# Performance work log

Hardware: AMD Instinct MI355X
Metric: run time of the kernel (lower is better)

Reference implementation:

```python
import jax, jax.numpy as jnp
from jax import lax
import numpy as np

B = 32768      # batch
D = 256        # input = hidden = output dim
DEPTH = 9      # universal_depth


def setup_inputs() -> dict:
    key = jax.random.key(0)
    ks = jax.random.split(key, 16)
    s = 1.0 / np.sqrt(D)  # keep pre-activations sane
    r = lambda k, shp, sc=s: (jax.random.normal(k, shp, jnp.float32) * sc)
    return {
        "x": jax.random.normal(ks[0], (B, D), jnp.float32),
        "lin0_w": r(ks[1], (D, D)), "lin0_b": r(ks[2], (D,), 0.1),
        "lin1_w": r(ks[3], (D, D)), "lin1_b": r(ks[4], (D,), 0.1),
        "u1_w": jax.random.normal(ks[5], (DEPTH, D, D), jnp.float32),
        "u1_cw": r(ks[6], (D, D)), "u1_cb": r(ks[7], (D,), 0.1),
        "lin2_w": r(ks[8], (D, D)), "lin2_b": r(ks[9], (D,), 0.1),
        "u2_w": jax.random.normal(ks[10], (DEPTH, D, D), jnp.float32),
        "u2_cw": r(ks[11], (D, D)), "u2_cb": r(ks[12], (D,), 0.1),
        "lino_w": r(ks[13], (D, D)), "lino_b": r(ks[14], (D,), 0.1),
    }


def _universal_layer(x, uw, cw, cb):
    """UniversalNeuralLayer.forward, vectorized.

    The circulant 'gate' matrix implements, for state s of length n:
        s'[i] = cos*s[i] - sin*s[(i+1)%n] + sin*s[(i-1)%n]
    Applied 3 times per depth with angles uw[d, j, 0..2] (j = output unit).
    The result is independent of x and of the batch index.
    """
    n = x.shape[1]
    classical = x @ cw + cb                      # [B, n]
    # angle sequence per output j, in (depth, gate) order -> [3*DEPTH, n]
    angles = jnp.transpose(uw[:, :, :3], (0, 2, 1)).reshape(-1, n)
    init = jnp.full((n, n), 1.0 / np.sqrt(n), dtype=x.dtype)  # [n_j, n_state]

    def step(s, ang):
        c = jnp.cos(ang)[:, None]
        sn = jnp.sin(ang)[:, None]
        return c * s + sn * (jnp.roll(s, 1, axis=1) - jnp.roll(s, -1, axis=1)), None

    s, _ = lax.scan(step, init, angles)
    p = s[:, 0] ** 2                             # |state[0]|^2 per output j
    return jnp.tanh(classical + p[None, :])


def reference(x, lin0_w, lin0_b, lin1_w, lin1_b, u1_w, u1_cw, u1_cb,
              lin2_w, lin2_b, u2_w, u2_cw, u2_cb, lino_w, lino_b):
    h = jax.nn.relu(x @ lin0_w.T + lin0_b)
    h = jax.nn.relu(h @ lin1_w.T + lin1_b)
    h = _universal_layer(h, u1_w, u1_cw, u1_cb)
    h = jax.nn.relu(h @ lin2_w.T + lin2_b)
    h = _universal_layer(h, u2_w, u2_cw, u2_cb)
    return jax.nn.relu(h @ lino_w.T + lino_b)
```

## Files before the change

kernel.cpp:

```cpp
#include <hip/hip_runtime.h>
#include <math.h>

#define DD 256

typedef float  f32x4  __attribute__((ext_vector_type(4)));
typedef short  bf16x8 __attribute__((ext_vector_type(8)));

__device__ __forceinline__ unsigned short f2bf(float f) {
    unsigned int u = __float_as_uint(f);
    u = (u + 0x7fffu + ((u >> 16) & 1u)) >> 16;
    return (unsigned short)u;
}
__device__ __forceinline__ float bf2f(unsigned int h16) {
    return __uint_as_float(h16 << 16);
}

__global__ __launch_bounds__(256)
void universal_p_kernel(const float* __restrict__ u1_w,
                        const float* __restrict__ u2_w,
                        float* __restrict__ p_out ) {
    const int j = threadIdx.x;
    const float* uw = blockIdx.x ? u2_w : u1_w;
    float s = 0.0625f;
#pragma unroll
    for (int d = 0; d < 9; ++d)
#pragma unroll
        for (int g = 0; g < 3; ++g)
            s *= cosf(uw[d * DD * DD + j * DD + g]);
    p_out[blockIdx.x * DD + j] = s * s;
}

__global__ __launch_bounds__(256)
void prep_weights(const float* __restrict__ w0, const float* __restrict__ w1,
                  const float* __restrict__ cw1, const float* __restrict__ w2,
                  const float* __restrict__ cw2, const float* __restrict__ wo,
                  unsigned short* __restrict__ wall) {
    const int gid  = blockIdx.x * 256 + threadIdx.x;
    const int mat  = gid >> 13;
    const int rem  = gid & 8191;
    const int wb   = rem >> 11;
    const int rem2 = rem & 2047;
    const int k0   = rem2 >> 8;
    const int rem3 = rem2 & 255;
    const int nt   = rem3 >> 6;
    const int lane = rem3 & 63;
    const int n  = wb * 64 + nt * 16 + (lane & 15);
    const int kb = k0 * 32 + (lane >> 4) * 8;

    const float* src;
    bool tr = false;
    switch (mat) {
        case 0: src = w0; break;
        case 1: src = w1; break;
        case 2: src = cw1; tr = true; break;
        case 3: src = w2; break;
        case 4: src = cw2; tr = true; break;
        default: src = wo; break;
    }
    unsigned short tmp[8];
#pragma unroll
    for (int j = 0; j < 8; ++j) {
        const float v = tr ? src[(kb + j) * DD + n] : src[n * DD + kb + j];
        tmp[j] = f2bf(v);
    }
    *(uint4*)&wall[mat * 65536 + wb * 16384 + k0 * 2048 + nt * 512 + lane * 8] =
        *(const uint4*)tmp;
}

__device__ __forceinline__ int chunk_idx(int m, int kc) {
    return kc * 32 + (m ^ (kc & 7));
}

__device__ __forceinline__ float fast_tanh(float x) {
    const float e = __expf(2.0f * x);
    return 1.0f - 2.0f * __builtin_amdgcn_rcpf(1.0f + e);
}

template <int MODE>
__device__ __forceinline__ void layer_step(uint4* h, bf16x8 (&wr)[2][4],
                                           const unsigned short* __restrict__ W,
                                           const unsigned short* __restrict__ Wn,
                                           const float* __restrict__ bias,
                                           const float* __restrict__ pv) {
    const int tid  = threadIdx.x;
    const int wave = tid >> 6;
    const int lane = tid & 63;
    const int quad = lane >> 4;
    const int l15  = lane & 15;
    const unsigned short* Wb  = W  + wave * 16384 + lane * 8;
    const unsigned short* Wnb = Wn + wave * 16384 + lane * 8;

    f32x4 acc[4][2];
#pragma unroll
    for (int nt = 0; nt < 4; ++nt)
#pragma unroll
        for (int mt = 0; mt < 2; ++mt) acc[nt][mt] = (f32x4){0.f, 0.f, 0.f, 0.f};

    bf16x8 h_f[2][2];
#pragma unroll
    for (int mt = 0; mt < 2; ++mt)
        h_f[0][mt] = *(const bf16x8*)&h[chunk_idx(mt * 16 + l15, quad)];

#pragma unroll
    for (int k0 = 0; k0 < 8; ++k0) {
        const int cur = k0 & 1, nxt = cur ^ 1;
        {
            const unsigned short* ws = (k0 < 7) ? &Wb[(k0 + 1) * 2048] : Wnb;
#pragma unroll
            for (int nt = 0; nt < 4; ++nt)
                wr[nxt][nt] = *(const bf16x8*)&ws[nt * 512];
        }
        if (k0 < 7) {
            const int kc = (k0 + 1) * 4 + quad;
#pragma unroll
            for (int mt = 0; mt < 2; ++mt)
                h_f[nxt][mt] = *(const bf16x8*)&h[chunk_idx(mt * 16 + l15, kc)];
        }
#pragma unroll
        for (int nt = 0; nt < 4; ++nt)
#pragma unroll
            for (int mt = 0; mt < 2; ++mt)
                acc[nt][mt] = __builtin_amdgcn_mfma_f32_16x16x32_bf16(
                    wr[cur][nt], h_f[cur][mt], acc[nt][mt], 0, 0, 0);
    }

    __syncthreads();

    const int nb = wave * 64;
#pragma unroll
    for (int nt = 0; nt < 4; ++nt) {
        const int n0 = nb + nt * 16 + quad * 4;
        f32x4 add = *(const f32x4*)&bias[n0];
        if (MODE == 1) add += *(const f32x4*)&pv[n0];
        const int kc_o = n0 >> 3;
        const int half = quad & 1;
#pragma unroll
        for (int mt = 0; mt < 2; ++mt) {
            const f32x4 v = acc[nt][mt] + add;
            float t0, t1, t2, t3;
            if (MODE == 1) {
                t0 = fast_tanh(v.x); t1 = fast_tanh(v.y);
                t2 = fast_tanh(v.z); t3 = fast_tanh(v.w);
            } else {
                t0 = fmaxf(v.x, 0.f); t1 = fmaxf(v.y, 0.f);
                t2 = fmaxf(v.z, 0.f); t3 = fmaxf(v.w, 0.f);
            }
            uint2 u;
            u.x = (unsigned int)f2bf(t0) | ((unsigned int)f2bf(t1) << 16);
            u.y = (unsigned int)f2bf(t2) | ((unsigned int)f2bf(t3) << 16);
            *(uint2*)((char*)&h[chunk_idx(mt * 16 + l15, kc_o)] + half * 8) = u;
        }
    }
    __syncthreads();
}

__global__ __launch_bounds__(256, 2)
void unet_fused(const float* __restrict__ x,
                const unsigned short* __restrict__ wall,
                const float* __restrict__ b0, const float* __restrict__ b1,
                const float* __restrict__ cb1, const float* __restrict__ b2,
                const float* __restrict__ cb2, const float* __restrict__ bo,
                const float* __restrict__ pbuf,
                float* __restrict__ out) {
    __shared__ uint4 h[1024];
    const int m0 = blockIdx.x * 32;
    const int tid = threadIdx.x;
    const int wave = tid >> 6;
    const int lane = tid & 63;

    bf16x8 wr[2][4];
    {
        const unsigned short* ws = wall + wave * 16384 + lane * 8;
#pragma unroll
        for (int nt = 0; nt < 4; ++nt)
            wr[0][nt] = *(const bf16x8*)&ws[nt * 512];
    }

    const int c4 = tid & 63;
    const int rbase = (tid >> 6) * 8;
    const int kc_s = c4 >> 1;
    const int half_s = c4 & 1;
#pragma unroll
    for (int i = 0; i < 8; ++i) {
        const int row = rbase + i;
        const float4 v = *(const float4*)&x[(size_t)(m0 + row) * DD + c4 * 4];
        uint2 u;
        u.x = (unsigned int)f2bf(v.x) | ((unsigned int)f2bf(v.y) << 16);
        u.y = (unsigned int)f2bf(v.z) | ((unsigned int)f2bf(v.w) << 16);
        *(uint2*)((char*)&h[chunk_idx(row, kc_s)] + half_s * 8) = u;
    }
    __syncthreads();

    layer_step<0>(h, wr, wall + 0 * 65536, wall + 1 * 65536, b0, nullptr);
    layer_step<0>(h, wr, wall + 1 * 65536, wall + 2 * 65536, b1, nullptr);
    layer_step<1>(h, wr, wall + 2 * 65536, wall + 3 * 65536, cb1, pbuf);
    layer_step<0>(h, wr, wall + 3 * 65536, wall + 4 * 65536, b2, nullptr);
    layer_step<1>(h, wr, wall + 4 * 65536, wall + 5 * 65536, cb2, pbuf + 256);
    layer_step<0>(h, wr, wall + 5 * 65536, wall + 0 * 65536, bo, nullptr);

#pragma unroll
    for (int i = 0; i < 8; ++i) {
        const int row = rbase + i;
        const uint2 u = *(const uint2*)((char*)&h[chunk_idx(row, kc_s)] + half_s * 8);
        float4 v;
        v.x = bf2f(u.x & 0xffffu); v.y = bf2f(u.x >> 16);
        v.z = bf2f(u.y & 0xffffu); v.w = bf2f(u.y >> 16);
        *(float4*)&out[(size_t)(m0 + row) * DD + c4 * 4] = v;
    }
}

extern "C" void kernel_launch(void* const* d_in, const int* in_sizes, int n_in,
                              void* d_out, int out_size, void* d_ws, size_t ws_size,
                              hipStream_t stream) {
    const float* x      = (const float*)d_in[0];
    const float* lin0_w = (const float*)d_in[1];
    const float* lin0_b = (const float*)d_in[2];
    const float* lin1_w = (const float*)d_in[3];
    const float* lin1_b = (const float*)d_in[4];
    const float* u1_w   = (const float*)d_in[5];
    const float* u1_cw  = (const float*)d_in[6];
    const float* u1_cb  = (const float*)d_in[7];
    const float* lin2_w = (const float*)d_in[8];
    const float* lin2_b = (const float*)d_in[9];
    const float* u2_w   = (const float*)d_in[10];
    const float* u2_cw  = (const float*)d_in[11];
    const float* u2_cb  = (const float*)d_in[12];
    const float* lino_w = (const float*)d_in[13];
    const float* lino_b = (const float*)d_in[14];

    float* out = (float*)d_out;
    unsigned short* wall = (unsigned short*)d_ws;
    float* pbuf = (float*)((char*)d_ws + 6 * 65536 * 2);

    universal_p_kernel<<<dim3(2), dim3(256), 0, stream>>>(u1_w, u2_w, pbuf);
    prep_weights<<<dim3(192), dim3(256), 0, stream>>>(
        lin0_w, lin1_w, u1_cw, lin2_w, u2_cw, lino_w, wall);
    unet_fused<<<dim3(1024), dim3(256), 0, stream>>>(
        x, wall, lin0_b, lin1_b, u1_cb, lin2_b, u2_cb, lino_b, pbuf, out);
}
```

Before: 153.1 us.

## Double-buffer activations in LDS and deepen weight register prefetch ring

Activations now alternate between two shared-memory buffers, so each layer reads one and writes the other, which removes one block barrier per layer. Weight fragments are prefetched two k-steps ahead through a three-slot register ring whose phase is carried across layers. The launch bound is raised to allow four blocks per CU for more latency hiding. This costs double the LDS and extra VGPRs, with a risk of spills or register pressure under the tighter bound.

```diff
diff --git a/kernel.cpp b/kernel.cpp
--- a/kernel.cpp
+++ b/kernel.cpp
@@ -76,8 +76,9 @@
     return 1.0f - 2.0f * __builtin_amdgcn_rcpf(1.0f + e);
 }
 
-template <int MODE>
-__device__ __forceinline__ void layer_step(uint4* h, bf16x8 (&wr)[2][4],
+template <int PHASE, int MODE>
+__device__ __forceinline__ void layer_step(const uint4* hc, uint4* hn,
+                                           bf16x8 (&wr)[3][4],
                                            const unsigned short* __restrict__ W,
                                            const unsigned short* __restrict__ Wn,
                                            const float* __restrict__ bias,
@@ -99,32 +100,33 @@
     bf16x8 h_f[2][2];
 #pragma unroll
     for (int mt = 0; mt < 2; ++mt)
-        h_f[0][mt] = *(const bf16x8*)&h[chunk_idx(mt * 16 + l15, quad)];
+        h_f[0][mt] = *(const bf16x8*)&hc[chunk_idx(mt * 16 + l15, quad)];
 
 #pragma unroll
     for (int k0 = 0; k0 < 8; ++k0) {
-        const int cur = k0 & 1, nxt = cur ^ 1;
+        const int cur = (PHASE + k0) % 3;
+        const int pf  = (PHASE + k0 + 2) % 3;
         {
-            const unsigned short* ws = (k0 < 7) ? &Wb[(k0 + 1) * 2048] : Wnb;
+            const unsigned short* ws =
+                (k0 < 6) ? &Wb[(k0 + 2) * 2048] : &Wnb[(k0 - 6) * 2048];
 #pragma unroll
             for (int nt = 0; nt < 4; ++nt)
-                wr[nxt][nt] = *(const bf16x8*)&ws[nt * 512];
+                wr[pf][nt] = *(const bf16x8*)&ws[nt * 512];
         }
         if (k0 < 7) {
             const int kc = (k0 + 1) * 4 + quad;
 #pragma unroll
             for (int mt = 0; mt < 2; ++mt)
-                h_f[nxt][mt] = *(const bf16x8*)&h[chunk_idx(mt * 16 + l15, kc)];
+                h_f[(k0 + 1) & 1][mt] =
+                    *(const bf16x8*)&hc[chunk_idx(mt * 16 + l15, kc)];
         }
 #pragma unroll
         for (int nt = 0; nt < 4; ++nt)
 #pragma unroll
             for (int mt = 0; mt < 2; ++mt)
                 acc[nt][mt] = __builtin_amdgcn_mfma_f32_16x16x32_bf16(
-                    wr[cur][nt], h_f[cur][mt], acc[nt][mt], 0, 0, 0);
-    }
-
-    __syncthreads();
+                    wr[cur][nt], h_f[k0 & 1][mt], acc[nt][mt], 0, 0, 0);
+    }
 
     const int nb = wave * 64;
 #pragma unroll
@@ -148,13 +150,13 @@
             uint2 u;
             u.x = (unsigned int)f2bf(t0) | ((unsigned int)f2bf(t1) << 16);
             u.y = (unsigned int)f2bf(t2) | ((unsigned int)f2bf(t3) << 16);
-            *(uint2*)((char*)&h[chunk_idx(mt * 16 + l15, kc_o)] + half * 8) = u;
+            *(uint2*)((char*)&hn[chunk_idx(mt * 16 + l15, kc_o)] + half * 8) = u;
         }
     }
     __syncthreads();
 }
 
-__global__ __launch_bounds__(256, 2)
+__global__ __launch_bounds__(256, 4)
 void unet_fused(const float* __restrict__ x,
                 const unsigned short* __restrict__ wall,
                 const float* __restrict__ b0, const float* __restrict__ b1,
@@ -162,18 +164,20 @@
                 const float* __restrict__ cb2, const float* __restrict__ bo,
                 const float* __restrict__ pbuf,
                 float* __restrict__ out) {
-    __shared__ uint4 h[1024];
+    __shared__ uint4 h[2][1024];
     const int m0 = blockIdx.x * 32;
     const int tid = threadIdx.x;
     const int wave = tid >> 6;
     const int lane = tid & 63;
 
-    bf16x8 wr[2][4];
+    bf16x8 wr[3][4];
     {
         const unsigned short* ws = wall + wave * 16384 + lane * 8;
 #pragma unroll
-        for (int nt = 0; nt < 4; ++nt)
+        for (int nt = 0; nt < 4; ++nt) {
             wr[0][nt] = *(const bf16x8*)&ws[nt * 512];
+            wr[1][nt] = *(const bf16x8*)&ws[2048 + nt * 512];
+        }
     }
 
     const int c4 = tid & 63;
@@ -187,21 +191,21 @@
         uint2 u;
         u.x = (unsigned int)f2bf(v.x) | ((unsigned int)f2bf(v.y) << 16);
         u.y = (unsigned int)f2bf(v.z) | ((unsigned int)f2bf(v.w) << 16);
-        *(uint2*)((char*)&h[chunk_idx(row, kc_s)] + half_s * 8) = u;
+        *(uint2*)((char*)&h[0][chunk_idx(row, kc_s)] + half_s * 8) = u;
     }
     __syncthreads();
 
-    layer_step<0>(h, wr, wall + 0 * 65536, wall + 1 * 65536, b0, nullptr);
-    layer_step<0>(h, wr, wall + 1 * 65536, wall + 2 * 65536, b1, nullptr);
-    layer_step<1>(h, wr, wall + 2 * 65536, wall + 3 * 65536, cb1, pbuf);
-    layer_step<0>(h, wr, wall + 3 * 65536, wall + 4 * 65536, b2, nullptr);
-    layer_step<1>(h, wr, wall + 4 * 65536, wall + 5 * 65536, cb2, pbuf + 256);
-    layer_step<0>(h, wr, wall + 5 * 65536, wall + 0 * 65536, bo, nullptr);
+    layer_step<0, 0>(h[0], h[1], wr, wall + 0 * 65536, wall + 1 * 65536, b0, nullptr);
+    layer_step<2, 0>(h[1], h[0], wr, wall + 1 * 65536, wall + 2 * 65536, b1, nullptr);
+    layer_step<1, 1>(h[0], h[1], wr, wall + 2 * 65536, wall + 3 * 65536, cb1, pbuf);
+    layer_step<0, 0>(h[1], h[0], wr, wall + 3 * 65536, wall + 4 * 65536, b2, nullptr);
+    layer_step<2, 1>(h[0], h[1], wr, wall + 4 * 65536, wall + 5 * 65536, cb2, pbuf + 256);
+    layer_step<1, 0>(h[1], h[0], wr, wall + 5 * 65536, wall + 0 * 65536, bo, nullptr);
 
 #pragma unroll
     for (int i = 0; i < 8; ++i) {
         const int row = rbase + i;
-        const uint2 u = *(const uint2*)((char*)&h[chunk_idx(row, kc_s)] + half_s * 8);
+        const uint2 u = *(const uint2*)((char*)&h[0][chunk_idx(row, kc_s)] + half_s * 8);
         float4 v;
         v.x = bf2f(u.x & 0xffffu); v.y = bf2f(u.x >> 16);
         v.z = bf2f(u.y & 0xffffu); v.w = bf2f(u.y >> 16);
```

Result: slower. 161.4 us (+5.4%).
